# Kernel optimization log

Measured on AMD Instinct MI355X. Metric: run time of the kernel, lower is better.

## Reference

```python
import math
import jax, jax.numpy as jnp
import numpy as np

H = 128
N_NODES = 20000
N_PAIRS = 160000
NB_NODE = 4
NB_EDGE = 4


def _build_graph(rng):
    u = rng.integers(0, N_NODES, N_PAIRS)
    v = (u + 1 + rng.integers(0, N_NODES - 1, N_PAIRS)) % N_NODES  # v != u
    src = np.concatenate([np.arange(N_NODES), u, v]).astype(np.int32)
    dst = np.concatenate([np.arange(N_NODES), v, u]).astype(np.int32)
    E = src.shape[0]
    # reverse-edge index: self-loops map to themselves, pair blocks swap
    rev = np.concatenate([np.arange(N_NODES),
                          N_NODES + N_PAIRS + np.arange(N_PAIRS),
                          N_NODES + np.arange(N_PAIRS)]).astype(np.int32)
    # slot of each edge inside its dst group (stable edge order), for to_dense_batch
    order = np.argsort(dst, kind='stable')
    counts = np.bincount(dst, minlength=N_NODES)
    starts = np.concatenate([[0], np.cumsum(counts)[:-1]])
    pos = np.arange(E) - starts[dst[order]]
    slot = np.empty(E, dtype=np.int32)
    slot[order] = pos.astype(np.int32)
    return src, dst, rev, slot, int(counts.max())


def setup_inputs() -> dict:
    rng = np.random.default_rng(0)
    src, dst, rev, slot, max_deg = _build_graph(rng)
    E = src.shape[0]
    key = jax.random.key(0)
    ks = jax.random.split(key, 16)
    s = 0.05
    W = lambda k, shape: jax.random.normal(k, shape, jnp.float32) * s
    return dict(
        node_states=jnp.asarray(rng.integers(0, 2, (N_NODES, NB_NODE)), jnp.int32),
        edge_states=jnp.asarray(rng.integers(0, 2, (E, NB_EDGE)), jnp.int32),
        scalars=jax.random.uniform(ks[0], (E, 1), jnp.float32),
        src_idx=jnp.asarray(src), dst_idx=jnp.asarray(dst),
        rev_idx=jnp.asarray(rev), slot_idx=jnp.asarray(slot),
        self_loop_idx=jnp.arange(N_NODES, dtype=jnp.int32),
        max_deg=max_deg,
        emb_v=W(ks[1], (2 ** (NB_NODE + 1), H)),
        emb_b=W(ks[2], (2 ** (NB_NODE + 1), H)),
        emb_e=W(ks[3], (2 ** NB_EDGE, H)),
        emb_s=W(ks[4], (4, H)),
        Wq=W(ks[5], (H, H)), Wk=W(ks[6], (H, H)), Wv=W(ks[7], (H, H)),
        Wek=W(ks[8], (H, H)), Wev=W(ks[9], (H, H)), Wcf=W(ks[10], (3 * H, H)),
        gW1=W(ks[11], (H, H)), gb1=jnp.zeros((H,), jnp.float32),
        gW2=W(ks[12], (H, 1)), gb2=jnp.zeros((1,), jnp.float32),
    )


def _from_binary(x):
    p = 2 ** jnp.arange(x.shape[-1], dtype=jnp.int32)
    return jnp.sum(x * p, axis=-1)


def _entmax15(logits):
    z = jnp.sort(logits, axis=-1)[..., ::-1]
    cz = jnp.cumsum(z, -1)
    cz2 = jnp.cumsum(z * z, -1)
    k = jnp.arange(1, z.shape[-1] + 1, dtype=logits.dtype)
    mz, mz2 = cz / k, cz2 / k
    discr = jax.nn.relu(mz * mz - mz2 + 1.0 / k)
    tau_c = mz - jnp.sqrt(discr)
    kidx = jnp.sum(z > tau_c, axis=-1, keepdims=True)
    tau = jnp.take_along_axis(tau_c, kidx - 1, axis=-1)
    r = jax.nn.relu(logits - tau)
    return r * r


def _sparsemax(logits):
    z = jnp.sort(logits, axis=-1)[..., ::-1]
    cz = jnp.cumsum(z, -1)
    k = jnp.arange(1, z.shape[-1] + 1, dtype=logits.dtype)
    support = k * z > cz - 1.0
    kidx = jnp.sum(support, axis=-1, keepdims=True)
    csk = jnp.take_along_axis(cz, kidx - 1, axis=-1)
    tau = (csk - 1.0) / kidx.astype(logits.dtype)
    return jax.nn.relu(logits - tau)


def reference(node_states, edge_states, scalars, src_idx, dst_idx, rev_idx,
              slot_idx, self_loop_idx, max_deg,
              emb_v, emb_b, emb_e, emb_s, Wq, Wk, Wv, Wek, Wev, Wcf,
              gW1, gb1, gW2, gb2):
    N = node_states.shape[0]
    h = Wq.shape[0]
    node_code = 2 * _from_binary(node_states)              # use_select_best=False
    node_fts = emb_v[node_code]                            # [N,h]
    edge_fts_emb = emb_e[_from_binary(edge_states)]        # [E,h]
    u = jax.nn.sigmoid(jax.nn.relu(node_fts @ gW1 + gb1) @ gW2 + gb2)  # [N,1]
    Q = node_fts @ Wq
    Kn = node_fts @ Wk
    Vn = node_fts @ Wv
    # combined edge K/V
    sel_best = emb_b[node_code[src_idx]]                   # [E,h]
    node_scalars = scalars[self_loop_idx]                  # [N,1] (self-loop edges)
    sender_s = node_scalars[src_idx]
    recv_s = node_scalars[dst_idx]
    rlx = (scalars < recv_s).astype(jnp.int32)
    rlx_d = (sender_s + scalars < recv_s).astype(jnp.int32)
    static_fts = emb_s[_from_binary(jnp.concatenate([rlx, rlx_d], axis=-1))]
    combined = jnp.concatenate([edge_fts_emb, edge_fts_emb[rev_idx], static_fts], -1) @ Wcf
    edge_K = sel_best @ Wek
    edge_V = combined @ Wev
    K_comb = Kn[src_idx] + edge_K                          # [E,h]
    V_comb = Vn[src_idx] + edge_V
    # to_dense_batch by dst
    dense_K = jnp.zeros((N, max_deg, h), K_comb.dtype).at[dst_idx, slot_idx].set(K_comb)
    dense_V = jnp.zeros((N, max_deg, h), V_comb.dtype).at[dst_idx, slot_idx].set(V_comb)
    mask = jnp.zeros((N, max_deg), bool).at[dst_idx, slot_idx].set(True)
    cK = jnp.concatenate([Kn[:, None], dense_K], axis=1)   # [N,1+max_deg,h]
    cV = jnp.concatenate([Vn[:, None], dense_V], axis=1)
    cmask = jnp.concatenate([jnp.ones((N, 1), bool), mask], axis=1)
    logits = jnp.einsum('nh,nmh->nm', Q, cK) / math.sqrt(h)
    logits = jnp.where(cmask, logits, jnp.asarray(-1e9, logits.dtype))
    p15 = _entmax15(logits)
    psoft = jax.nn.softmax(logits, axis=-1)
    psp = _sparsemax(logits)
    w_low = u * 2.0
    w_high = (u - 0.5) * 2.0
    probs = jnp.where(u <= 0.5,
                      (1.0 - w_low) * psoft + w_low * p15,
                      (1.0 - w_high) * p15 + w_high * psp)
    is_sel = (probs > 1e-6).astype(probs.dtype)
    hard = is_sel / (jnp.sum(is_sel, axis=1, keepdims=True) + 1e-9)
    attn = jax.lax.stop_gradient(hard - probs) + probs     # straight-through
    attn = attn * cmask.astype(attn.dtype)
    agg = jnp.einsum('nm,nmh->nh', attn, cV)
    node_out = node_fts + agg
    edge_out = edge_fts_emb + agg[dst_idx]
    return node_out, edge_out
```

## Files before the change

kernel.cpp:

```cpp
#include <hip/hip_runtime.h>

#define H 128
#define MAXD 64

__global__ __launch_bounds__(128) void k_tables1(
    const float* __restrict__ emb_v, const float* __restrict__ emb_b,
    const float* __restrict__ emb_e, const float* __restrict__ emb_s,
    const float* __restrict__ Wq, const float* __restrict__ Wk,
    const float* __restrict__ Wv, const float* __restrict__ Wek,
    const float* __restrict__ Wcf,
    const float* __restrict__ gW1, const float* __restrict__ gb1,
    const float* __restrict__ gW2, const float* __restrict__ gb2,
    float* __restrict__ Qc, float* __restrict__ Knc, float* __restrict__ Vnc,
    float* __restrict__ KEc, float* __restrict__ tmpA, float* __restrict__ tmpB,
    float* __restrict__ tmpC, float* __restrict__ uc)
{
    int b = blockIdx.x;
    int j = threadIdx.x;
    if (b < 32) {
        int c = b;
        float acc = 0.f;
        for (int k = 0; k < H; ++k) acc += emb_v[c*H + k] * Wq[k*H + j];
        Qc[c*H + j] = acc;
    } else if (b < 64) {
        int c = b - 32;
        float acc = 0.f;
        for (int k = 0; k < H; ++k) acc += emb_v[c*H + k] * Wk[k*H + j];
        Knc[c*H + j] = acc;
    } else if (b < 96) {
        int c = b - 64;
        float acc = 0.f;
        for (int k = 0; k < H; ++k) acc += emb_v[c*H + k] * Wv[k*H + j];
        Vnc[c*H + j] = acc;
    } else if (b < 128) {
        int c = b - 96;
        float acc = 0.f;
        for (int k = 0; k < H; ++k)
            acc += emb_v[c*H + k] * Wk[k*H + j] + emb_b[c*H + k] * Wek[k*H + j];
        KEc[c*H + j] = acc;
    } else if (b < 144) {
        int c = b - 128;
        float acc = 0.f;
        for (int k = 0; k < H; ++k) acc += emb_e[c*H + k] * Wcf[k*H + j];
        tmpA[c*H + j] = acc;
    } else if (b < 160) {
        int c = b - 144;
        float acc = 0.f;
        for (int k = 0; k < H; ++k) acc += emb_e[c*H + k] * Wcf[(H + k)*H + j];
        tmpB[c*H + j] = acc;
    } else if (b < 164) {
        int c = b - 160;
        float acc = 0.f;
        for (int k = 0; k < H; ++k) acc += emb_s[c*H + k] * Wcf[(2*H + k)*H + j];
        tmpC[c*H + j] = acc;
    } else {
        int c = b - 164;
        float acc = 0.f;
        for (int k = 0; k < H; ++k) acc += emb_v[c*H + k] * gW1[k*H + j];
        float hj = fmaxf(acc + gb1[j], 0.f) * gW2[j];
        __shared__ float sb[2];
        float v = hj;
        for (int off = 32; off; off >>= 1) v += __shfl_xor(v, off);
        if ((threadIdx.x & 63) == 0) sb[threadIdx.x >> 6] = v;
        __syncthreads();
        if (threadIdx.x == 0) {
            float x = sb[0] + sb[1] + gb2[0];
            uc[c] = 1.f / (1.f + expf(-x));
        }
    }
}

__global__ __launch_bounds__(128) void k_tables2(
    const float* __restrict__ Wev,
    const float* __restrict__ tmpA, const float* __restrict__ tmpB,
    const float* __restrict__ tmpC,
    const float* __restrict__ Qc, const float* __restrict__ Knc,
    const float* __restrict__ KEc,
    float* __restrict__ Ae, float* __restrict__ Be, float* __restrict__ Cs,
    float* __restrict__ Ldot, float* __restrict__ Lself)
{
    int b = blockIdx.x;
    int j = threadIdx.x;
    const float scale = 1.0f / 11.313708498984761f;
    if (b < 16) {
        float acc = 0.f;
        for (int k = 0; k < H; ++k) acc += tmpA[b*H + k] * Wev[k*H + j];
        Ae[b*H + j] = acc;
    } else if (b < 32) {
        int c = b - 16;
        float acc = 0.f;
        for (int k = 0; k < H; ++k) acc += tmpB[c*H + k] * Wev[k*H + j];
        Be[c*H + j] = acc;
    } else if (b < 36) {
        int c = b - 32;
        float acc = 0.f;
        for (int k = 0; k < H; ++k) acc += tmpC[c*H + k] * Wev[k*H + j];
        Cs[c*H + j] = acc;
    } else {
        int a = b - 36;
        float qj = Qc[a*H + j];
        __shared__ float sb[2];
        for (int bb = 0; bb < 32; ++bb) {
            float v = qj * KEc[bb*H + j];
            for (int off = 32; off; off >>= 1) v += __shfl_xor(v, off);
            if ((threadIdx.x & 63) == 0) sb[threadIdx.x >> 6] = v;
            __syncthreads();
            if (threadIdx.x == 0) Ldot[a*32 + bb] = (sb[0] + sb[1]) * scale;
            __syncthreads();
        }
        float v = qj * Knc[a*H + j];
        for (int off = 32; off; off >>= 1) v += __shfl_xor(v, off);
        if ((threadIdx.x & 63) == 0) sb[threadIdx.x >> 6] = v;
        __syncthreads();
        if (threadIdx.x == 0) Lself[a] = (sb[0] + sb[1]) * scale;
    }
}

__global__ __launch_bounds__(256) void k_nodecode(
    const int* __restrict__ ns, int* __restrict__ node_code, int N)
{
    int t = blockIdx.x * 256 + threadIdx.x;
    if (t < N)
        node_code[t] = 2 * (ns[4*t] + 2*ns[4*t+1] + 4*ns[4*t+2] + 8*ns[4*t+3]);
}

__global__ __launch_bounds__(256) void k_edgeprep(
    const int* __restrict__ edge_states, const float* __restrict__ scalars,
    const int* __restrict__ src_idx, const int* __restrict__ dst_idx,
    const int* __restrict__ rev_idx, const int* __restrict__ slot_idx,
    const int* __restrict__ self_loop, const int* __restrict__ node_code,
    int* __restrict__ ecode, int* __restrict__ adjP, int* __restrict__ deg, int E)
{
    int e = blockIdx.x * 256 + threadIdx.x;
    if (e >= E) return;
    int ec = edge_states[4*e] + 2*edge_states[4*e+1] + 4*edge_states[4*e+2] + 8*edge_states[4*e+3];
    ecode[e] = ec;
    int rv = rev_idx[e];
    int er = edge_states[4*rv] + 2*edge_states[4*rv+1] + 4*edge_states[4*rv+2] + 8*edge_states[4*rv+3];
    float se = scalars[e];
    int sn = src_idx[e], dn = dst_idx[e];
    float ss = scalars[self_loop[sn]];
    float rs = scalars[self_loop[dn]];
    int rlx  = (se < rs) ? 1 : 0;
    int rlxd = ((ss + se) < rs) ? 1 : 0;
    int sc = rlx + 2 * rlxd;
    int cs = node_code[sn];
    int packed = cs | (ec << 5) | (er << 9) | (sc << 13);
    int sl = slot_idx[e];
    if (sl < MAXD) adjP[(size_t)dn * MAXD + sl] = packed;
    atomicAdd(&deg[dn], 1);
}

__global__ __launch_bounds__(256) void k_attn(
    const int* __restrict__ node_code, const int* __restrict__ deg,
    const int* __restrict__ adjP, const float* __restrict__ uc,
    const float* __restrict__ Lself, const float* __restrict__ Ldot,
    const float* __restrict__ Vnc, const float* __restrict__ Ae,
    const float* __restrict__ Be, const float* __restrict__ Cs,
    const float* __restrict__ emb_v,
    float* __restrict__ agg, float* __restrict__ node_out, int N)
{
    __shared__ float sortbuf[4][64];
    int lane = threadIdx.x & 63;
    int w = threadIdx.x >> 6;
    int n = blockIdx.x * 4 + w;
    bool valid = n < N;
    int cn = 0, d = 0;
    if (valid) {
        cn = node_code[n];
        d = deg[n];
        if (d > 63) d = 63;
    }

    float z = -1e9f;
    int padj = 0;
    if (valid) {
        if (lane == 0) z = Lself[cn];
        else if (lane <= d) {
            padj = adjP[(size_t)n * MAXD + lane - 1];
            z = Ldot[cn * 32 + (padj & 31)];
        }
    }

    int rank = 0;
    for (int jj = 0; jj < 64; ++jj) {
        float zj = __shfl(z, jj);
        rank += (zj > z) || (zj == z && jj < lane);
    }
    sortbuf[w][rank] = z;
    __syncthreads();
    float zs = sortbuf[w][lane];

    float cz = zs, cz2 = zs * zs;
    for (int off = 1; off < 64; off <<= 1) {
        float a = __shfl_up(cz, off);
        float b = __shfl_up(cz2, off);
        if (lane >= off) { cz += a; cz2 += b; }
    }

    float kk = (float)(lane + 1);
    float mz = cz / kk, mz2 = cz2 / kk;
    float discr = fmaxf(mz * mz - mz2 + 1.0f / kk, 0.0f);
    float tau_c = mz - sqrtf(discr);
    int kidx = __popcll(__ballot(zs > tau_c));
    float tau15 = __shfl(tau_c, kidx - 1);
    float r15 = fmaxf(z - tau15, 0.0f);
    float p15 = r15 * r15;

    int ksp = __popcll(__ballot(kk * zs > cz - 1.0f));
    float csk = __shfl(cz, ksp - 1);
    float tausp = (csk - 1.0f) / (float)ksp;
    float psp = fmaxf(z - tausp, 0.0f);

    float zmax = __shfl(zs, 0);
    float ex = expf(z - zmax);
    float s = ex;
    for (int off = 32; off; off >>= 1) s += __shfl_xor(s, off);
    float psoft = ex / s;

    float uu = uc[cn];
    float probs;
    if (uu <= 0.5f) { float wl = 2.0f * uu;         probs = (1.0f - wl) * psoft + wl * p15; }
    else            { float wh = (uu - 0.5f) * 2.0f; probs = (1.0f - wh) * p15 + wh * psp; }

    unsigned long long msk = __ballot(probs > 1e-6f);
    int cnt = __popcll(msk);
    float scale = 1.0f / ((float)cnt + 1e-9f);

    float a0 = 0.f, a1 = 0.f;
    unsigned long long mk = msk;
    while (mk) {
        int sl = __ffsll(mk) - 1;
        mk &= mk - 1;
        if (sl == 0) {
            a0 += Vnc[cn*H + lane];
            a1 += Vnc[cn*H + 64 + lane];
        } else {
            int p = __shfl(padj, sl);
            int cs = p & 31, ec = (p >> 5) & 15, er = (p >> 9) & 15, sc = (p >> 13) & 3;
            a0 += Vnc[cs*H + lane]      + Ae[ec*H + lane]      + Be[er*H + lane]      + Cs[sc*H + lane];
            a1 += Vnc[cs*H + 64 + lane] + Ae[ec*H + 64 + lane] + Be[er*H + 64 + lane] + Cs[sc*H + 64 + lane];
        }
    }
    a0 *= scale; a1 *= scale;

    if (valid) {
        agg[(size_t)n*H + lane]      = a0;
        agg[(size_t)n*H + 64 + lane] = a1;
        node_out[(size_t)n*H + lane]      = emb_v[cn*H + lane]      + a0;
        node_out[(size_t)n*H + 64 + lane] = emb_v[cn*H + 64 + lane] + a1;
    }
}

__global__ __launch_bounds__(256) void k_edgeout(
    const int* __restrict__ ecode, const int* __restrict__ dst_idx,
    const float* __restrict__ agg, const float* __restrict__ emb_e,
    float* __restrict__ out_edge, int E)
{
    long long t = (long long)blockIdx.x * 256 + threadIdx.x;
    if (t >= (long long)E * 32) return;
    int e = (int)(t >> 5);
    int q = (int)(t & 31);
    int ec = ecode[e];
    int dn = dst_idx[e];
    float4 ve = ((const float4*)(emb_e + (size_t)ec * H))[q];
    float4 va = ((const float4*)(agg + (size_t)dn * H))[q];
    float4 r;
    r.x = ve.x + va.x; r.y = ve.y + va.y; r.z = ve.z + va.z; r.w = ve.w + va.w;
    ((float4*)(out_edge + (size_t)e * H))[q] = r;
}

extern "C" void kernel_launch(void* const* d_in, const int* in_sizes, int n_in,
                              void* d_out, int out_size, void* d_ws, size_t ws_size,
                              hipStream_t stream)
{
    const int*   node_states = (const int*)d_in[0];
    const int*   edge_states = (const int*)d_in[1];
    const float* scalars     = (const float*)d_in[2];
    const int*   src_idx     = (const int*)d_in[3];
    const int*   dst_idx     = (const int*)d_in[4];
    const int*   rev_idx     = (const int*)d_in[5];
    const int*   slot_idx    = (const int*)d_in[6];
    const int*   self_loop   = (const int*)d_in[7];
    const float* emb_v = (const float*)d_in[9];
    const float* emb_b = (const float*)d_in[10];
    const float* emb_e = (const float*)d_in[11];
    const float* emb_s = (const float*)d_in[12];
    const float* Wq  = (const float*)d_in[13];
    const float* Wk  = (const float*)d_in[14];
    const float* Wv  = (const float*)d_in[15];
    const float* Wek = (const float*)d_in[16];
    const float* Wev = (const float*)d_in[17];
    const float* Wcf = (const float*)d_in[18];
    const float* gW1 = (const float*)d_in[19];
    const float* gb1 = (const float*)d_in[20];
    const float* gW2 = (const float*)d_in[21];
    const float* gb2 = (const float*)d_in[22];

    const int N = in_sizes[0] / 4;
    const int E = in_sizes[1] / 4;

    float* ws   = (float*)d_ws;
    float* Qc   = ws; ws += 32*H;
    float* Knc  = ws; ws += 32*H;
    float* Vnc  = ws; ws += 32*H;
    float* KEc  = ws; ws += 32*H;
    float* tmpA = ws; ws += 16*H;
    float* tmpB = ws; ws += 16*H;
    float* tmpC = ws; ws += 4*H;
    float* Ae   = ws; ws += 16*H;
    float* Be   = ws; ws += 16*H;
    float* Cs   = ws; ws += 4*H;
    float* uc   = ws; ws += 32;
    float* Lself= ws; ws += 32;
    float* Ldot = ws; ws += 32*32;
    float* agg  = ws; ws += (size_t)N*H;
    int* node_code = (int*)ws;
    int* ecode = node_code + N;
    int* adjP  = ecode + E;
    int* deg   = adjP + (size_t)N * MAXD;

    hipMemsetAsync(deg, 0, (size_t)N * sizeof(int), stream);

    k_tables1<<<196, 128, 0, stream>>>(emb_v, emb_b, emb_e, emb_s, Wq, Wk, Wv, Wek,
                                       Wcf, gW1, gb1, gW2, gb2,
                                       Qc, Knc, Vnc, KEc, tmpA, tmpB, tmpC, uc);
    k_tables2<<<68, 128, 0, stream>>>(Wev, tmpA, tmpB, tmpC, Qc, Knc, KEc,
                                      Ae, Be, Cs, Ldot, Lself);
    k_nodecode<<<(N + 255) / 256, 256, 0, stream>>>(node_states, node_code, N);
    k_edgeprep<<<(E + 255) / 256, 256, 0, stream>>>(edge_states, scalars, src_idx,
                                                    dst_idx, rev_idx, slot_idx,
                                                    self_loop, node_code,
                                                    ecode, adjP, deg, E);
    k_attn<<<(N + 3) / 4, 256, 0, stream>>>(node_code, deg, adjP, uc, Lself, Ldot,
                                            Vnc, Ae, Be, Cs, emb_v,
                                            agg, (float*)d_out, N);
    long long tot = (long long)E * 32;
    k_edgeout<<<(int)((tot + 255) / 256), 256, 0, stream>>>(ecode, dst_idx, agg, emb_e,
                                                            (float*)d_out + (size_t)N * H, E);
}
```

Baseline: 341.6 us.

## Fuse edge output into attention kernel and stage lookup tables in LDS

Edge outputs are now written directly from the attention kernel, which iterates each node's adjacency list using a new per-slot edge-id array. This removes the separate edge-output pass and the agg buffer round trip. The degree atomics are replaced by a 0xFF memset sentinel on adjP, and node-code computation is merged into the table kernel. The small V/A/B/C/emb_e tables are copied into shared memory on each block, and loads are vectorized. The trade-offs are an extra adjacency-sized memset and adjE writes, per-block table staging, and scattered edge-output stores, some of which are nontemporal.

```diff
diff --git a/kernel.cpp b/kernel.cpp
--- a/kernel.cpp
+++ b/kernel.cpp
@@ -2,6 +2,8 @@
 
 #define H 128
 #define MAXD 64
+
+typedef float nfloat2 __attribute__((ext_vector_type(2)));
 
 __global__ __launch_bounds__(128) void k_tables1(
     const float* __restrict__ emb_v, const float* __restrict__ emb_b,
@@ -11,9 +13,11 @@
     const float* __restrict__ Wcf,
     const float* __restrict__ gW1, const float* __restrict__ gb1,
     const float* __restrict__ gW2, const float* __restrict__ gb2,
+    const int* __restrict__ node_states,
     float* __restrict__ Qc, float* __restrict__ Knc, float* __restrict__ Vnc,
     float* __restrict__ KEc, float* __restrict__ tmpA, float* __restrict__ tmpB,
-    float* __restrict__ tmpC, float* __restrict__ uc)
+    float* __restrict__ tmpC, float* __restrict__ uc,
+    int* __restrict__ node_code, int N)
 {
     int b = blockIdx.x;
     int j = threadIdx.x;
@@ -53,7 +57,7 @@
         float acc = 0.f;
         for (int k = 0; k < H; ++k) acc += emb_s[c*H + k] * Wcf[(2*H + k)*H + j];
         tmpC[c*H + j] = acc;
-    } else {
+    } else if (b < 196) {
         int c = b - 164;
         float acc = 0.f;
         for (int k = 0; k < H; ++k) acc += emb_v[c*H + k] * gW1[k*H + j];
@@ -65,7 +69,13 @@
         __syncthreads();
         if (threadIdx.x == 0) {
             float x = sb[0] + sb[1] + gb2[0];
-            uc[c] = 1.f / (1.f + expf(-x));
+            uc[c] = 1.f / (1.f + __expf(-x));
+        }
+    } else {
+        int t = (b - 196) * 128 + j;
+        if (t < N) {
+            int4 ns = ((const int4*)node_states)[t];
+            node_code[t] = 2 * (ns.x + 2*ns.y + 4*ns.z + 8*ns.w);
         }
     }
 }
@@ -116,71 +126,83 @@
     }
 }
 
-__global__ __launch_bounds__(256) void k_nodecode(
-    const int* __restrict__ ns, int* __restrict__ node_code, int N)
-{
-    int t = blockIdx.x * 256 + threadIdx.x;
-    if (t < N)
-        node_code[t] = 2 * (ns[4*t] + 2*ns[4*t+1] + 4*ns[4*t+2] + 8*ns[4*t+3]);
-}
-
 __global__ __launch_bounds__(256) void k_edgeprep(
     const int* __restrict__ edge_states, const float* __restrict__ scalars,
     const int* __restrict__ src_idx, const int* __restrict__ dst_idx,
     const int* __restrict__ rev_idx, const int* __restrict__ slot_idx,
     const int* __restrict__ self_loop, const int* __restrict__ node_code,
-    int* __restrict__ ecode, int* __restrict__ adjP, int* __restrict__ deg, int E)
+    int* __restrict__ adjP, int* __restrict__ adjE, int E)
 {
     int e = blockIdx.x * 256 + threadIdx.x;
     if (e >= E) return;
-    int ec = edge_states[4*e] + 2*edge_states[4*e+1] + 4*edge_states[4*e+2] + 8*edge_states[4*e+3];
-    ecode[e] = ec;
+    int4 es = ((const int4*)edge_states)[e];
+    int ec = es.x + 2*es.y + 4*es.z + 8*es.w;
     int rv = rev_idx[e];
-    int er = edge_states[4*rv] + 2*edge_states[4*rv+1] + 4*edge_states[4*rv+2] + 8*edge_states[4*rv+3];
+    int4 er4 = ((const int4*)edge_states)[rv];
+    int er = er4.x + 2*er4.y + 4*er4.z + 8*er4.w;
     float se = scalars[e];
     int sn = src_idx[e], dn = dst_idx[e];
     float ss = scalars[self_loop[sn]];
     float rs = scalars[self_loop[dn]];
-    int rlx  = (se < rs) ? 1 : 0;
-    int rlxd = ((ss + se) < rs) ? 1 : 0;
-    int sc = rlx + 2 * rlxd;
+    int sc = ((se < rs) ? 1 : 0) + 2 * (((ss + se) < rs) ? 1 : 0);
     int cs = node_code[sn];
     int packed = cs | (ec << 5) | (er << 9) | (sc << 13);
     int sl = slot_idx[e];
-    if (sl < MAXD) adjP[(size_t)dn * MAXD + sl] = packed;
-    atomicAdd(&deg[dn], 1);
-}
+    if (sl < MAXD) {
+        adjP[(size_t)dn * MAXD + sl] = packed;
+        adjE[(size_t)dn * MAXD + sl] = e;
+    }
+}
+
+#define ROWS_V 0
+#define ROWS_A 32
+#define ROWS_B 48
+#define ROWS_C 64
+#define ROWS_E 68
+#define ROWS_T 84
 
 __global__ __launch_bounds__(256) void k_attn(
-    const int* __restrict__ node_code, const int* __restrict__ deg,
-    const int* __restrict__ adjP, const float* __restrict__ uc,
+    const int* __restrict__ node_code, const int* __restrict__ adjP,
+    const int* __restrict__ adjE, const float* __restrict__ uc,
     const float* __restrict__ Lself, const float* __restrict__ Ldot,
     const float* __restrict__ Vnc, const float* __restrict__ Ae,
     const float* __restrict__ Be, const float* __restrict__ Cs,
-    const float* __restrict__ emb_v,
-    float* __restrict__ agg, float* __restrict__ node_out, int N)
-{
+    const float* __restrict__ emb_e, const float* __restrict__ emb_v,
+    float* __restrict__ node_out, float* __restrict__ edge_out, int N)
+{
+    __shared__ float tbl[ROWS_T * H];
     __shared__ float sortbuf[4][64];
-    int lane = threadIdx.x & 63;
-    int w = threadIdx.x >> 6;
+    int tid = threadIdx.x;
+
+    {
+        float4* t4 = (float4*)tbl;
+        const float4* s;
+        s = (const float4*)Vnc;   for (int i = tid; i < 32*H/4; i += 256) t4[ROWS_V*H/4 + i] = s[i];
+        s = (const float4*)Ae;    for (int i = tid; i < 16*H/4; i += 256) t4[ROWS_A*H/4 + i] = s[i];
+        s = (const float4*)Be;    for (int i = tid; i < 16*H/4; i += 256) t4[ROWS_B*H/4 + i] = s[i];
+        s = (const float4*)Cs;    for (int i = tid; i <  4*H/4; i += 256) t4[ROWS_C*H/4 + i] = s[i];
+        s = (const float4*)emb_e; for (int i = tid; i < 16*H/4; i += 256) t4[ROWS_E*H/4 + i] = s[i];
+    }
+
+    int lane = tid & 63;
+    int w = tid >> 6;
     int n = blockIdx.x * 4 + w;
     bool valid = n < N;
-    int cn = 0, d = 0;
-    if (valid) {
-        cn = node_code[n];
-        d = deg[n];
-        if (d > 63) d = 63;
-    }
-
+    int cn = 0;
+    if (valid) cn = node_code[n];
+
+    int padj = -1, eid = 0;
+    if (valid && lane >= 1) {
+        padj = adjP[(size_t)n * MAXD + lane - 1];
+        if (padj != -1) eid = adjE[(size_t)n * MAXD + lane - 1];
+    }
     float z = -1e9f;
-    int padj = 0;
     if (valid) {
         if (lane == 0) z = Lself[cn];
-        else if (lane <= d) {
-            padj = adjP[(size_t)n * MAXD + lane - 1];
-            z = Ldot[cn * 32 + (padj & 31)];
-        }
-    }
+        else if (padj != -1) z = Ldot[cn * 32 + (padj & 31)];
+    }
+
+    __syncthreads();
 
     int rank = 0;
     for (int jj = 0; jj < 64; ++jj) {
@@ -213,61 +235,57 @@
     float psp = fmaxf(z - tausp, 0.0f);
 
     float zmax = __shfl(zs, 0);
-    float ex = expf(z - zmax);
+    float ex = __expf(z - zmax);
     float s = ex;
     for (int off = 32; off; off >>= 1) s += __shfl_xor(s, off);
     float psoft = ex / s;
 
     float uu = uc[cn];
     float probs;
-    if (uu <= 0.5f) { float wl = 2.0f * uu;         probs = (1.0f - wl) * psoft + wl * p15; }
+    if (uu <= 0.5f) { float wl = 2.0f * uu;          probs = (1.0f - wl) * psoft + wl * p15; }
     else            { float wh = (uu - 0.5f) * 2.0f; probs = (1.0f - wh) * p15 + wh * psp; }
 
-    unsigned long long msk = __ballot(probs > 1e-6f);
+    unsigned long long msk = valid ? __ballot(probs > 1e-6f) : 0ull;
     int cnt = __popcll(msk);
     float scale = 1.0f / ((float)cnt + 1e-9f);
 
-    float a0 = 0.f, a1 = 0.f;
+    const float2* t2 = (const float2*)tbl;
+    float ax = 0.f, ay = 0.f;
     unsigned long long mk = msk;
     while (mk) {
         int sl = __ffsll(mk) - 1;
         mk &= mk - 1;
         if (sl == 0) {
-            a0 += Vnc[cn*H + lane];
-            a1 += Vnc[cn*H + 64 + lane];
+            float2 v = t2[(ROWS_V + cn) * 64 + lane];
+            ax += v.x; ay += v.y;
         } else {
             int p = __shfl(padj, sl);
-            int cs = p & 31, ec = (p >> 5) & 15, er = (p >> 9) & 15, sc = (p >> 13) & 3;
-            a0 += Vnc[cs*H + lane]      + Ae[ec*H + lane]      + Be[er*H + lane]      + Cs[sc*H + lane];
-            a1 += Vnc[cs*H + 64 + lane] + Ae[ec*H + 64 + lane] + Be[er*H + 64 + lane] + Cs[sc*H + 64 + lane];
+            float2 v  = t2[(ROWS_V + (p & 31)) * 64 + lane];
+            float2 va = t2[(ROWS_A + ((p >> 5) & 15)) * 64 + lane];
+            float2 vb = t2[(ROWS_B + ((p >> 9) & 15)) * 64 + lane];
+            float2 vc = t2[(ROWS_C + ((p >> 13) & 3)) * 64 + lane];
+            ax += v.x + va.x + vb.x + vc.x;
+            ay += v.y + va.y + vb.y + vc.y;
         }
     }
-    a0 *= scale; a1 *= scale;
+    ax *= scale; ay *= scale;
 
     if (valid) {
-        agg[(size_t)n*H + lane]      = a0;
-        agg[(size_t)n*H + 64 + lane] = a1;
-        node_out[(size_t)n*H + lane]      = emb_v[cn*H + lane]      + a0;
-        node_out[(size_t)n*H + 64 + lane] = emb_v[cn*H + 64 + lane] + a1;
-    }
-}
-
-__global__ __launch_bounds__(256) void k_edgeout(
-    const int* __restrict__ ecode, const int* __restrict__ dst_idx,
-    const float* __restrict__ agg, const float* __restrict__ emb_e,
-    float* __restrict__ out_edge, int E)
-{
-    long long t = (long long)blockIdx.x * 256 + threadIdx.x;
-    if (t >= (long long)E * 32) return;
-    int e = (int)(t >> 5);
-    int q = (int)(t & 31);
-    int ec = ecode[e];
-    int dn = dst_idx[e];
-    float4 ve = ((const float4*)(emb_e + (size_t)ec * H))[q];
-    float4 va = ((const float4*)(agg + (size_t)dn * H))[q];
-    float4 r;
-    r.x = ve.x + va.x; r.y = ve.y + va.y; r.z = ve.z + va.z; r.w = ve.w + va.w;
-    ((float4*)(out_edge + (size_t)e * H))[q] = r;
+        float2 ev = ((const float2*)emb_v)[cn * 64 + lane];
+        float2 r; r.x = ev.x + ax; r.y = ev.y + ay;
+        ((float2*)node_out)[(size_t)n * 64 + lane] = r;
+    }
+
+    unsigned long long vm = valid ? __ballot(padj != -1) : 0ull;
+    while (vm) {
+        int sl = __ffsll(vm) - 1;
+        vm &= vm - 1;
+        int e = __shfl(eid, sl);
+        int p = __shfl(padj, sl);
+        float2 ee = t2[(ROWS_E + ((p >> 5) & 15)) * 64 + lane];
+        nfloat2 r; r.x = ee.x + ax; r.y = ee.y + ay;
+        __builtin_nontemporal_store(r, (nfloat2*)edge_out + (size_t)e * 64 + lane);
+    }
 }
 
 extern "C" void kernel_launch(void* const* d_in, const int* in_sizes, int n_in,
@@ -314,28 +332,25 @@
     float* uc   = ws; ws += 32;
     float* Lself= ws; ws += 32;
     float* Ldot = ws; ws += 32*32;
-    float* agg  = ws; ws += (size_t)N*H;
     int* node_code = (int*)ws;
-    int* ecode = node_code + N;
-    int* adjP  = ecode + E;
-    int* deg   = adjP + (size_t)N * MAXD;
-
-    hipMemsetAsync(deg, 0, (size_t)N * sizeof(int), stream);
-
-    k_tables1<<<196, 128, 0, stream>>>(emb_v, emb_b, emb_e, emb_s, Wq, Wk, Wv, Wek,
-                                       Wcf, gW1, gb1, gW2, gb2,
-                                       Qc, Knc, Vnc, KEc, tmpA, tmpB, tmpC, uc);
+    int* adjP  = node_code + N;
+    int* adjE  = adjP + (size_t)N * MAXD;
+
+    (void)hipMemsetAsync(adjP, 0xFF, (size_t)N * MAXD * sizeof(int), stream);
+
+    int ncb = (N + 127) / 128;
+    k_tables1<<<196 + ncb, 128, 0, stream>>>(emb_v, emb_b, emb_e, emb_s, Wq, Wk, Wv, Wek,
+                                             Wcf, gW1, gb1, gW2, gb2, node_states,
+                                             Qc, Knc, Vnc, KEc, tmpA, tmpB, tmpC, uc,
+                                             node_code, N);
     k_tables2<<<68, 128, 0, stream>>>(Wev, tmpA, tmpB, tmpC, Qc, Knc, KEc,
                                       Ae, Be, Cs, Ldot, Lself);
-    k_nodecode<<<(N + 255) / 256, 256, 0, stream>>>(node_states, node_code, N);
     k_edgeprep<<<(E + 255) / 256, 256, 0, stream>>>(edge_states, scalars, src_idx,
                                                     dst_idx, rev_idx, slot_idx,
                                                     self_loop, node_code,
-                                                    ecode, adjP, deg, E);
-    k_attn<<<(N + 3) / 4, 256, 0, stream>>>(node_code, deg, adjP, uc, Lself, Ldot,
-                                            Vnc, Ae, Be, Cs, emb_v,
-                                            agg, (float*)d_out, N);
-    long long tot = (long long)E * 32;
-    k_edgeout<<<(int)((tot + 255) / 256), 256, 0, stream>>>(ecode, dst_idx, agg, emb_e,
-                                                            (float*)d_out + (size_t)N * H, E);
-}
+                                                    adjP, adjE, E);
+    k_attn<<<(N + 3) / 4, 256, 0, stream>>>(node_code, adjP, adjE, uc, Lself, Ldot,
+                                            Vnc, Ae, Be, Cs, emb_e, emb_v,
+                                            (float*)d_out,
+                                            (float*)d_out + (size_t)N * H, N);
+}
```

After: 348.9 us. +2.1%, slower.
